# Performance work log

Measured on AMD Instinct MI355X. Metric: run time of the kernel, lower is better.

The kernel has to match this reference:

```python
import jax, jax.numpy as jnp
import numpy as np

EMB_DIM = 64
B, S, D = 64, 1024, 64

def setup_inputs() -> dict:
    key = jax.random.key(0)
    k1, k2, k3, k4, k5 = jax.random.split(key, 5)
    return {
        "query": jax.random.normal(k1, (B, S, D), dtype=jnp.float32),
        "key": jax.random.normal(k2, (B, S, D), dtype=jnp.float32),
        "value": jax.random.normal(k3, (B, S, D), dtype=jnp.float32),
        "a_key": jax.random.normal(k4, (S, S, D), dtype=jnp.float32),
        "a_value": jax.random.normal(k5, (S, S, D), dtype=jnp.float32),
    }

def reference(query, key, value, a_key, a_value):
    scale = jnp.sqrt(jnp.asarray(EMB_DIM, dtype=query.dtype))
    # standard content-content scores: [B, Sq, Sk]
    qk = jnp.einsum("bqd,bkd->bqk", query, key)
    # relative key scores: a_key is [Sq, Sk, D]; contract over D per query position
    rel_qk = jnp.einsum("bqd,qkd->bqk", query, a_key)
    attn = jax.nn.softmax((qk + rel_qk) / scale, axis=-1)
    # content values + relative values
    qkv = jnp.einsum("bqk,bkd->bqd", attn, value)
    rel_qkv = jnp.einsum("bqk,qkd->bqd", attn, a_value)
    return qkv + rel_qkv, attn
```

## Files before the change

kernel.cpp:

```cpp
#include <hip/hip_runtime.h>
#include <stdint.h>

#define S_ 1024
#define D_ 64
#define B_ 64

typedef short short8 __attribute__((ext_vector_type(8)));
typedef unsigned short ushort8 __attribute__((ext_vector_type(8)));
typedef float f32x4 __attribute__((ext_vector_type(4)));
typedef unsigned short u16;

__device__ __forceinline__ u16 f2bf(float x) {
    uint32_t u = __builtin_bit_cast(uint32_t, x);
    return (u16)((u + 0x7FFFu + ((u >> 16) & 1u)) >> 16);
}
__device__ __forceinline__ float bf2f(u16 b) {
    return __builtin_bit_cast(float, ((uint32_t)b) << 16);
}
__device__ __forceinline__ uint32_t pack2(float a, float b) {
    return (uint32_t)f2bf(a) | ((uint32_t)f2bf(b) << 16);
}
__device__ __forceinline__ int scidx(int row, int k) {
    return (((row << 10) + (k & ~7)) ^ ((row & 15) << 3)) + (k & 7);
}

template <int WS>
__global__ __launch_bounds__(256) void k1_qk(const float* __restrict__ Q,
                                             const float* __restrict__ Kk,
                                             float* __restrict__ qkf,
                                             u16* __restrict__ qkb) {
    __shared__ __align__(16) u16 Qs[128][72];
    __shared__ __align__(16) u16 Ks[128][72];
    const float SCL = 0.18033688011112042f;
    const int bx = blockIdx.x;
    const int b  = bx >> 6;
    const int q0 = ((bx >> 3) & 7) << 7;
    const int k0 = (bx & 7) << 7;
    const int t  = threadIdx.x;
#pragma unroll
    for (int i = 0; i < 8; ++i) {
        int f = (i << 8) + t;
        int row = f >> 4, c = (f & 15) << 2;
        float4 v = *reinterpret_cast<const float4*>(&Q[((size_t)(b * S_ + q0 + row) << 6) + c]);
        *reinterpret_cast<uint2*>(&Qs[row][c]) = make_uint2(pack2(v.x, v.y), pack2(v.z, v.w));
        float4 u = *reinterpret_cast<const float4*>(&Kk[((size_t)(b * S_ + k0 + row) << 6) + c]);
        *reinterpret_cast<uint2*>(&Ks[row][c]) = make_uint2(pack2(u.x, u.y), pack2(u.z, u.w));
    }
    __syncthreads();
    const int l = t & 63, w = t >> 6, lr = l & 15, lg = l >> 4;
    short8 a[2][2];
#pragma unroll
    for (int mi = 0; mi < 2; ++mi)
#pragma unroll
        for (int h = 0; h < 2; ++h)
            a[mi][h] = *reinterpret_cast<const short8*>(&Qs[((w * 2 + mi) << 4) + lr][h * 32 + lg * 8]);
    f32x4 acc[2][8] = {};
#pragma unroll
    for (int n = 0; n < 8; ++n) {
        short8 b0 = *reinterpret_cast<const short8*>(&Ks[(n << 4) + lr][lg * 8]);
        short8 b1 = *reinterpret_cast<const short8*>(&Ks[(n << 4) + lr][32 + lg * 8]);
#pragma unroll
        for (int mi = 0; mi < 2; ++mi) {
            acc[mi][n] = __builtin_amdgcn_mfma_f32_16x16x32_bf16(a[mi][0], b0, acc[mi][n], 0, 0, 0);
            acc[mi][n] = __builtin_amdgcn_mfma_f32_16x16x32_bf16(a[mi][1], b1, acc[mi][n], 0, 0, 0);
        }
    }
#pragma unroll
    for (int mi = 0; mi < 2; ++mi)
#pragma unroll
        for (int n = 0; n < 8; ++n)
#pragma unroll
            for (int r = 0; r < 4; ++r) {
                int qq = q0 + ((w * 2 + mi) << 4) + (lg << 2) + r;
                int kc = k0 + (n << 4) + lr;
                size_t idx = ((size_t)(b * S_ + qq) << 10) + kc;
                if (WS) qkb[idx] = f2bf(acc[mi][n][r] * SCL);
                else    qkf[idx] = acc[mi][n][r] * SCL;
            }
}

__device__ __forceinline__ void tpose_store_p(u16* Tls, int pitch, float4 p,
                                              int kb, int t) {
    const int l = t & 63, lr = l & 15, lg = l >> 4;
    float v0 = p.x, v1 = p.y, v2 = p.z, v3 = p.w;
    float y0 = __shfl_xor(v0, 16), y1 = __shfl_xor(v1, 16),
          y2 = __shfl_xor(v2, 16), y3 = __shfl_xor(v3, 16);
    bool o = (lg & 1);
    float n0 = o ? y1 : v0, n1 = o ? v1 : y0, n2 = o ? y3 : v2, n3 = o ? v3 : y2;
    float z0 = __shfl_xor(n0, 32), z1 = __shfl_xor(n1, 32),
          z2 = __shfl_xor(n2, 32), z3 = __shfl_xor(n3, 32);
    bool h = (lg & 2);
    float T0 = h ? z2 : n0, T1 = h ? z3 : n1, T2 = h ? n2 : z0, T3 = h ? n3 : z1;
    int d = (lr << 2) + lg;
    *reinterpret_cast<uint2*>(&Tls[d * pitch + kb]) = make_uint2(pack2(T0, T1), pack2(T2, T3));
}

template <int WS>
__global__ __launch_bounds__(512) void k2_mid(const float* __restrict__ Q,
                                              const float* __restrict__ AK,
                                              const float* __restrict__ AV,
                                              u16* __restrict__ qkb,
                                              const float* __restrict__ qkf,
                                              float* __restrict__ invg,
                                              float* __restrict__ attn,
                                              float* __restrict__ outp) {
    __shared__ __align__(16) u16 Sc[64 * 1024];
    __shared__ __align__(16) u16 Qs[64][72];
    __shared__ __align__(16) u16 Ak[2][64][72];
    __shared__ float invs[64];
    const float SCL = 0.18033688011112042f;
    const int q = blockIdx.x;
    const int t = threadIdx.x;
    const int l = t & 63, w = t >> 6, lr = l & 15, lg = l >> 4;
    const int wq = w & 3;
    const int wh = w >> 2;
    const int srow = t >> 3, sc8 = (t & 7) << 3;

    {
        const float* qp = &Q[((size_t)(srow * S_ + q) << 6) + sc8];
        float4 a = *reinterpret_cast<const float4*>(qp);
        float4 b = *reinterpret_cast<const float4*>(qp + 4);
        *reinterpret_cast<uint4*>(&Qs[srow][sc8]) =
            make_uint4(pack2(a.x * SCL, a.y * SCL), pack2(a.z * SCL, a.w * SCL),
                       pack2(b.x * SCL, b.y * SCL), pack2(b.z * SCL, b.w * SCL));
    }
    const float* akbase = &AK[(size_t)q << 16];
    float4 pa[2][2];
#define LDK(set, tile) do { const float* p_ = akbase + ((size_t)(tile) << 12) + (srow << 6) + sc8; \
        pa[set][0] = *reinterpret_cast<const float4*>(p_);                                         \
        pa[set][1] = *reinterpret_cast<const float4*>(p_ + 4); } while (0)
#define STAGEK(buf) do {                                                                     \
        *reinterpret_cast<uint4*>(&Ak[buf][srow][sc8]) =                                     \
            make_uint4(pack2(pa[buf][0].x, pa[buf][0].y), pack2(pa[buf][0].z, pa[buf][0].w), \
                       pack2(pa[buf][1].x, pa[buf][1].y), pack2(pa[buf][1].z, pa[buf][1].w)); } while (0)
    LDK(0, 0); LDK(1, 1);
    __syncthreads();
    short8 qa[2][2];
#pragma unroll
    for (int bh = 0; bh < 2; ++bh)
#pragma unroll
        for (int h = 0; h < 2; ++h)
            qa[bh][h] = *reinterpret_cast<const short8*>(
                &Qs[(wh << 5) + (bh << 4) + lr][(h << 5) + (lg << 3)]);
    STAGEK(0);
    __syncthreads();

#pragma unroll 2
    for (int tt = 0; tt < 16; ++tt) {
        const int cur = tt & 1, nxt = cur ^ 1;
        short8 ak0 = *reinterpret_cast<const short8*>(&Ak[cur][(wq << 4) + lr][lg << 3]);
        short8 ak1 = *reinterpret_cast<const short8*>(&Ak[cur][(wq << 4) + lr][32 + (lg << 3)]);
        if (tt < 15) STAGEK(nxt);
        if (tt < 14) LDK(cur, tt + 2);
        int kbase = (tt << 6) + (wq << 4) + (lg << 2);
#pragma unroll
        for (int bh = 0; bh < 2; ++bh) {
            f32x4 c = {};
            c = __builtin_amdgcn_mfma_f32_16x16x32_bf16(ak0, qa[bh][0], c, 0, 0, 0);
            c = __builtin_amdgcn_mfma_f32_16x16x32_bf16(ak1, qa[bh][1], c, 0, 0, 0);
            *reinterpret_cast<uint2*>(&Sc[scidx((wh << 5) + (bh << 4) + lr, kbase)]) =
                make_uint2(pack2(c[0], c[1]), pack2(c[2], c[3]));
        }
        __syncthreads();
    }
#undef LDK
#undef STAGEK

    const float* avbase = &AV[(size_t)q << 16];
    float4 pv[2][2];
#pragma unroll
    for (int s = 0; s < 2; ++s)
#pragma unroll
        for (int i = 0; i < 2; ++i) {
            int f = (i << 9) + t;
            pv[s][i] = *reinterpret_cast<const float4*>(
                &avbase[((size_t)s << 12) + ((size_t)(f >> 4) << 6) + ((f & 15) << 2)]);
        }

    {
        const int ch = t & 7;
        float s = 0.f;
#pragma unroll 4
        for (int i = 0; i < 16; ++i) {
            int k = (((i << 3) + ch) << 3);
            int idx = scidx(srow, k);
            ushort8 rel = *reinterpret_cast<const ushort8*>(&Sc[idx]);
            float g[8];
            if (WS) {
                ushort8 gq = *reinterpret_cast<const ushort8*>(
                    &qkb[((size_t)(srow * S_ + q) << 10) + k]);
#pragma unroll
                for (int jj = 0; jj < 8; ++jj) g[jj] = bf2f(gq[jj]);
            } else {
                const float* qkrow = &qkf[((size_t)(srow * S_ + q) << 10)];
                float4 g0 = *reinterpret_cast<const float4*>(&qkrow[k]);
                float4 g1 = *reinterpret_cast<const float4*>(&qkrow[k + 4]);
                g[0] = g0.x; g[1] = g0.y; g[2] = g0.z; g[3] = g0.w;
                g[4] = g1.x; g[5] = g1.y; g[6] = g1.z; g[7] = g1.w;
            }
            ushort8 e;
#pragma unroll
            for (int jj = 0; jj < 8; ++jj) {
                float ev = exp2f(g[jj] + bf2f(rel[jj]));
                s += ev;
                e[jj] = f2bf(ev);
            }
            *reinterpret_cast<ushort8*>(&Sc[idx]) = e;
            if (WS)
                *reinterpret_cast<ushort8*>(&qkb[((size_t)(srow * S_ + q) << 10) + k]) = e;
        }
        s += __shfl_xor(s, 1); s += __shfl_xor(s, 2); s += __shfl_xor(s, 4);
        if (ch == 0) {
            float inv = 1.0f / s;
            invs[srow] = inv;
            if (WS) invg[srow * S_ + q] = inv;
        }
    }
    __syncthreads();

    tpose_store_p(&Ak[0][0][0], 72, pv[0][0], (w << 2), t);
    tpose_store_p(&Ak[0][0][0], 72, pv[0][1], 32 + (w << 2), t);
    __syncthreads();

    f32x4 oacc[2] = {};
#pragma unroll 2
    for (int tt = 0; tt < 16; ++tt) {
        const int cur = tt & 1, nxt = cur ^ 1;
        short8 bb0 = *reinterpret_cast<const short8*>(&Ak[cur][(wq << 4) + lr][lg << 3]);
        short8 bb1 = *reinterpret_cast<const short8*>(&Ak[cur][(wq << 4) + lr][32 + (lg << 3)]);
        if (tt < 15) {
            tpose_store_p(&Ak[nxt][0][0], 72, pv[nxt][0], (w << 2), t);
            tpose_store_p(&Ak[nxt][0][0], 72, pv[nxt][1], 32 + (w << 2), t);
        }
        if (tt < 14) {
#pragma unroll
            for (int i = 0; i < 2; ++i) {
                int f = (i << 9) + t;
                pv[cur][i] = *reinterpret_cast<const float4*>(
                    &avbase[((size_t)(tt + 2) << 12) + ((size_t)(f >> 4) << 6) + ((f & 15) << 2)]);
            }
        }
        {
            int col = (t & 255) << 2;
#pragma unroll
            for (int rr = 0; rr < 2; ++rr) {
                int row = (tt << 2) + (rr << 1) + (t >> 8);
                uint2 u = *reinterpret_cast<const uint2*>(&Sc[scidx(row, col)]);
                float inv = invs[row];
                float4 o = make_float4(bf2f((u16)(u.x & 0xffff)) * inv,
                                       bf2f((u16)(u.x >> 16)) * inv,
                                       bf2f((u16)(u.y & 0xffff)) * inv,
                                       bf2f((u16)(u.y >> 16)) * inv);
                *reinterpret_cast<float4*>(&attn[((size_t)(row * S_ + q) << 10) + col]) = o;
            }
        }
#pragma unroll
        for (int mi = 0; mi < 2; ++mi) {
            short8 ea0 = *reinterpret_cast<const short8*>(
                &Sc[scidx((wh << 5) + (mi << 4) + lr, (tt << 6) + (lg << 3))]);
            short8 ea1 = *reinterpret_cast<const short8*>(
                &Sc[scidx((wh << 5) + (mi << 4) + lr, (tt << 6) + 32 + (lg << 3))]);
            oacc[mi] = __builtin_amdgcn_mfma_f32_16x16x32_bf16(ea0, bb0, oacc[mi], 0, 0, 0);
            oacc[mi] = __builtin_amdgcn_mfma_f32_16x16x32_bf16(ea1, bb1, oacc[mi], 0, 0, 0);
        }
        __syncthreads();
    }
#pragma unroll
    for (int mi = 0; mi < 2; ++mi)
#pragma unroll
        for (int r = 0; r < 4; ++r) {
            int brow = (wh << 5) + (mi << 4) + (lg << 2) + r;
            outp[((size_t)(brow * S_ + q) << 6) + (wq << 4) + lr] = oacc[mi][r] * invs[brow];
        }
}

template <int WS>
__global__ __launch_bounds__(512) void k3_pv(const float* __restrict__ V,
                                             const float* __restrict__ attn,
                                             const u16* __restrict__ P,
                                             const float* __restrict__ invg,
                                             float* __restrict__ outp) {
    __shared__ __align__(16) u16 Vt[64 * 1032];
    __shared__ __align__(16) u16 At[2][64][72];
    const int b  = blockIdx.x >> 2;
    const int qq = blockIdx.x & 3;
    const int t  = threadIdx.x;
    const int l = t & 63, w = t >> 6, lr = l & 15, lg = l >> 4;
    const int wq = w & 3;
    const int dh = w >> 2;
    const int srow = t >> 3, sc8 = (t & 7) << 3;

    for (int kt = 0; kt < 16; ++kt) {
#pragma unroll
        for (int i = 0; i < 2; ++i) {
            int f = (i << 9) + t;
            int row = f >> 4, c = (f & 15) << 2;
            float4 pvv = *reinterpret_cast<const float4*>(
                &V[((size_t)(b * S_ + (kt << 6) + row) << 6) + c]);
            tpose_store_p(&Vt[0], 1032, pvv, (kt << 6) + (i << 5) + (w << 2), t);
        }
    }
    __syncthreads();

    for (int qs = 0; qs < 4; ++qs) {
        const int qsbase = (qq << 8) + (qs << 6);
        f32x4 acc[2] = {};
        if (WS) {
            const u16* prow = &P[((size_t)(b * S_ + qsbase + (wq << 4) + lr) << 10) + (lg << 3)];
            short8 a0b[2], a1b[2];
#define LDPB(buf, kt) do { const u16* p_ = prow + ((kt) << 6);              \
            a0b[buf] = *reinterpret_cast<const short8*>(p_);                \
            a1b[buf] = *reinterpret_cast<const short8*>(p_ + 32); } while (0)
            LDPB(0, 0); LDPB(1, 1);
#pragma unroll 2
            for (int kt = 0; kt < 16; ++kt) {
                const int buf = kt & 1;
                short8 a0 = a0b[buf], a1 = a1b[buf];
                if (kt < 14) LDPB(buf, kt + 2);
#pragma unroll
                for (int n = 0; n < 2; ++n) {
                    const u16* vb = &Vt[((dh << 5) + (n << 4) + lr) * 1032 + (kt << 6) + (lg << 3)];
                    short8 b0 = *reinterpret_cast<const short8*>(vb);
                    short8 b1 = *reinterpret_cast<const short8*>(vb + 32);
                    acc[n] = __builtin_amdgcn_mfma_f32_16x16x32_bf16(a0, b0, acc[n], 0, 0, 0);
                    acc[n] = __builtin_amdgcn_mfma_f32_16x16x32_bf16(a1, b1, acc[n], 0, 0, 0);
                }
            }
#undef LDPB
            float4 inv4 = *reinterpret_cast<const float4*>(
                &invg[b * S_ + qsbase + (wq << 4) + (lg << 2)]);
            float invr[4] = {inv4.x, inv4.y, inv4.z, inv4.w};
#pragma unroll
            for (int n = 0; n < 2; ++n)
#pragma unroll
                for (int r = 0; r < 4; ++r) {
                    size_t idx = ((size_t)(b * S_ + qsbase + (wq << 4) + (lg << 2) + r) << 6)
                                 + (dh << 5) + (n << 4) + lr;
                    outp[idx] += acc[n][r] * invr[r];
                }
        } else {
            const float* arow = &attn[((size_t)(b * S_ + qsbase + srow) << 10) + sc8];
            float4 pa[2][2];
#define LDA3(set, tile) do { const float* p_ = arow + ((tile) << 6);       \
            pa[set][0] = *reinterpret_cast<const float4*>(p_);             \
            pa[set][1] = *reinterpret_cast<const float4*>(p_ + 4); } while (0)
#define STAGEA(buf) do {                                                                     \
            *reinterpret_cast<uint4*>(&At[buf][srow][sc8]) =                                 \
                make_uint4(pack2(pa[buf][0].x, pa[buf][0].y), pack2(pa[buf][0].z, pa[buf][0].w), \
                           pack2(pa[buf][1].x, pa[buf][1].y), pack2(pa[buf][1].z, pa[buf][1].w)); } while (0)
            LDA3(0, 0); LDA3(1, 1);
            __syncthreads();
            STAGEA(0);
            __syncthreads();
#pragma unroll 2
            for (int kt = 0; kt < 16; ++kt) {
                const int cur = kt & 1, nxt = cur ^ 1;
                short8 a0 = *reinterpret_cast<const short8*>(&At[cur][(wq << 4) + lr][lg << 3]);
                short8 a1 = *reinterpret_cast<const short8*>(&At[cur][(wq << 4) + lr][32 + (lg << 3)]);
                if (kt < 15) STAGEA(nxt);
                if (kt < 14) LDA3(cur, kt + 2);
#pragma unroll
                for (int n = 0; n < 2; ++n) {
                    const u16* vb = &Vt[((dh << 5) + (n << 4) + lr) * 1032 + (kt << 6) + (lg << 3)];
                    short8 b0 = *reinterpret_cast<const short8*>(vb);
                    short8 b1 = *reinterpret_cast<const short8*>(vb + 32);
                    acc[n] = __builtin_amdgcn_mfma_f32_16x16x32_bf16(a0, b0, acc[n], 0, 0, 0);
                    acc[n] = __builtin_amdgcn_mfma_f32_16x16x32_bf16(a1, b1, acc[n], 0, 0, 0);
                }
                __syncthreads();
            }
#undef LDA3
#undef STAGEA
#pragma unroll
            for (int n = 0; n < 2; ++n)
#pragma unroll
                for (int r = 0; r < 4; ++r) {
                    size_t idx = ((size_t)(b * S_ + qsbase + (wq << 4) + (lg << 2) + r) << 6)
                                 + (dh << 5) + (n << 4) + lr;
                    outp[idx] += acc[n][r];
                }
        }
    }
}

extern "C" void kernel_launch(void* const* d_in, const int* in_sizes, int n_in,
                              void* d_out, int out_size, void* d_ws, size_t ws_size,
                              hipStream_t stream) {
    (void)in_sizes; (void)n_in; (void)out_size;
    const float* Q  = (const float*)d_in[0];
    const float* K  = (const float*)d_in[1];
    const float* V  = (const float*)d_in[2];
    const float* AK = (const float*)d_in[3];
    const float* AV = (const float*)d_in[4];
    float* outp = (float*)d_out;
    float* attn = outp + (size_t)B_ * S_ * D_;
    u16*   qkb  = (u16*)d_ws;
    float* invg = (float*)(qkb + (size_t)B_ * S_ * S_);
    const size_t need = (size_t)B_ * S_ * S_ * sizeof(u16)
                      + (size_t)B_ * S_ * sizeof(float);

    if (ws_size >= need) {
        k1_qk<1> <<<dim3(64 * 8 * 8), dim3(256), 0, stream>>>(Q, K, attn, qkb);
        k2_mid<1><<<dim3(1024),       dim3(512), 0, stream>>>(Q, AK, AV, qkb, attn, invg, attn, outp);
        k3_pv<1> <<<dim3(256),        dim3(512), 0, stream>>>(V, attn, qkb, invg, outp);
    } else {
        k1_qk<0> <<<dim3(64 * 8 * 8), dim3(256), 0, stream>>>(Q, K, attn, qkb);
        k2_mid<0><<<dim3(1024),       dim3(512), 0, stream>>>(Q, AK, AV, qkb, attn, invg, attn, outp);
        k3_pv<0> <<<dim3(256),        dim3(512), 0, stream>>>(V, attn, qkb, invg, outp);
    }
}
```

Before: 343.7 us.

## Split k2_mid across batch halves with XCD-aware block mapping and smaller blocks

k2_mid now runs 2048 blocks of 256 threads, each handling 32 batch rows for one query position instead of all 64. The block index is remapped so the two blocks sharing a query's a_key/a_value slab land on the same XCD, which should let the second read hit in L2. Shared memory per block is halved and the double-buffered a_key/a_value staging is replaced by a single buffer with an extra sync per tile. This should raise occupancy and spread work more evenly, at the cost of reading each relative-position slab twice and exposing more load latency in the loops.

```diff
diff --git a/kernel.cpp b/kernel.cpp
--- a/kernel.cpp
+++ b/kernel.cpp
@@ -96,7 +96,7 @@
 }
 
 template <int WS>
-__global__ __launch_bounds__(512) void k2_mid(const float* __restrict__ Q,
+__global__ __launch_bounds__(256) void k2_mid(const float* __restrict__ Q,
                                               const float* __restrict__ AK,
                                               const float* __restrict__ AV,
                                               u16* __restrict__ qkb,
@@ -104,20 +104,22 @@
                                               float* __restrict__ invg,
                                               float* __restrict__ attn,
                                               float* __restrict__ outp) {
-    __shared__ __align__(16) u16 Sc[64 * 1024];
-    __shared__ __align__(16) u16 Qs[64][72];
-    __shared__ __align__(16) u16 Ak[2][64][72];
-    __shared__ float invs[64];
+    __shared__ __align__(16) u16 Sc[32 * 1024];
+    __shared__ __align__(16) u16 Qs[32][72];
+    __shared__ __align__(16) u16 Ak[64][72];
+    __shared__ float invs[32];
     const float SCL = 0.18033688011112042f;
-    const int q = blockIdx.x;
+    const int j = blockIdx.x;
+    const int xcd = j & 7, slot = j >> 3;
+    const int q  = xcd * 128 + (slot >> 1);
+    const int b0 = (slot & 1) << 5;
     const int t = threadIdx.x;
     const int l = t & 63, w = t >> 6, lr = l & 15, lg = l >> 4;
-    const int wq = w & 3;
-    const int wh = w >> 2;
     const int srow = t >> 3, sc8 = (t & 7) << 3;
+    const int arow = t >> 2, acol = (t & 3) << 4;
 
     {
-        const float* qp = &Q[((size_t)(srow * S_ + q) << 6) + sc8];
+        const float* qp = &Q[((size_t)((b0 + srow) * S_ + q) << 6) + sc8];
         float4 a = *reinterpret_cast<const float4*>(qp);
         float4 b = *reinterpret_cast<const float4*>(qp + 4);
         *reinterpret_cast<uint4*>(&Qs[srow][sc8]) =
@@ -125,15 +127,20 @@
                        pack2(b.x * SCL, b.y * SCL), pack2(b.z * SCL, b.w * SCL));
     }
     const float* akbase = &AK[(size_t)q << 16];
-    float4 pa[2][2];
-#define LDK(set, tile) do { const float* p_ = akbase + ((size_t)(tile) << 12) + (srow << 6) + sc8; \
-        pa[set][0] = *reinterpret_cast<const float4*>(p_);                                         \
-        pa[set][1] = *reinterpret_cast<const float4*>(p_ + 4); } while (0)
-#define STAGEK(buf) do {                                                                     \
-        *reinterpret_cast<uint4*>(&Ak[buf][srow][sc8]) =                                     \
-            make_uint4(pack2(pa[buf][0].x, pa[buf][0].y), pack2(pa[buf][0].z, pa[buf][0].w), \
-                       pack2(pa[buf][1].x, pa[buf][1].y), pack2(pa[buf][1].z, pa[buf][1].w)); } while (0)
-    LDK(0, 0); LDK(1, 1);
+    float4 pa[4];
+#define LDK(tile) do { const float* p_ = akbase + ((size_t)(tile) << 12) + (arow << 6) + acol; \
+        pa[0] = *reinterpret_cast<const float4*>(p_);                                          \
+        pa[1] = *reinterpret_cast<const float4*>(p_ + 4);                                      \
+        pa[2] = *reinterpret_cast<const float4*>(p_ + 8);                                      \
+        pa[3] = *reinterpret_cast<const float4*>(p_ + 12); } while (0)
+#define STAGEK() do {                                                                        \
+        *reinterpret_cast<uint4*>(&Ak[arow][acol]) =                                         \
+            make_uint4(pack2(pa[0].x, pa[0].y), pack2(pa[0].z, pa[0].w),                     \
+                       pack2(pa[1].x, pa[1].y), pack2(pa[1].z, pa[1].w));                    \
+        *reinterpret_cast<uint4*>(&Ak[arow][acol + 8]) =                                     \
+            make_uint4(pack2(pa[2].x, pa[2].y), pack2(pa[2].z, pa[2].w),                     \
+                       pack2(pa[3].x, pa[3].y), pack2(pa[3].z, pa[3].w)); } while (0)
+    LDK(0);
     __syncthreads();
     short8 qa[2][2];
 #pragma unroll
@@ -141,24 +148,21 @@
 #pragma unroll
         for (int h = 0; h < 2; ++h)
             qa[bh][h] = *reinterpret_cast<const short8*>(
-                &Qs[(wh << 5) + (bh << 4) + lr][(h << 5) + (lg << 3)]);
-    STAGEK(0);
-    __syncthreads();
-
-#pragma unroll 2
+                &Qs[(bh << 4) + lr][(h << 5) + (lg << 3)]);
+
     for (int tt = 0; tt < 16; ++tt) {
-        const int cur = tt & 1, nxt = cur ^ 1;
-        short8 ak0 = *reinterpret_cast<const short8*>(&Ak[cur][(wq << 4) + lr][lg << 3]);
-        short8 ak1 = *reinterpret_cast<const short8*>(&Ak[cur][(wq << 4) + lr][32 + (lg << 3)]);
-        if (tt < 15) STAGEK(nxt);
-        if (tt < 14) LDK(cur, tt + 2);
-        int kbase = (tt << 6) + (wq << 4) + (lg << 2);
+        STAGEK();
+        __syncthreads();
+        if (tt < 15) LDK(tt + 1);
+        short8 ak0 = *reinterpret_cast<const short8*>(&Ak[(w << 4) + lr][lg << 3]);
+        short8 ak1 = *reinterpret_cast<const short8*>(&Ak[(w << 4) + lr][32 + (lg << 3)]);
+        int kbase = (tt << 6) + (w << 4) + (lg << 2);
 #pragma unroll
         for (int bh = 0; bh < 2; ++bh) {
             f32x4 c = {};
             c = __builtin_amdgcn_mfma_f32_16x16x32_bf16(ak0, qa[bh][0], c, 0, 0, 0);
             c = __builtin_amdgcn_mfma_f32_16x16x32_bf16(ak1, qa[bh][1], c, 0, 0, 0);
-            *reinterpret_cast<uint2*>(&Sc[scidx((wh << 5) + (bh << 4) + lr, kbase)]) =
+            *reinterpret_cast<uint2*>(&Sc[scidx((bh << 4) + lr, kbase)]) =
                 make_uint2(pack2(c[0], c[1]), pack2(c[2], c[3]));
         }
         __syncthreads();
@@ -167,15 +171,13 @@
 #undef STAGEK
 
     const float* avbase = &AV[(size_t)q << 16];
-    float4 pv[2][2];
-#pragma unroll
-    for (int s = 0; s < 2; ++s)
-#pragma unroll
-        for (int i = 0; i < 2; ++i) {
-            int f = (i << 9) + t;
-            pv[s][i] = *reinterpret_cast<const float4*>(
-                &avbase[((size_t)s << 12) + ((size_t)(f >> 4) << 6) + ((f & 15) << 2)]);
-        }
+    float4 pv[4];
+#pragma unroll
+    for (int i = 0; i < 4; ++i) {
+        int f = (i << 8) + t;
+        pv[i] = *reinterpret_cast<const float4*>(
+            &avbase[((size_t)(f >> 4) << 6) + ((f & 15) << 2)]);
+    }
 
     {
         const int ch = t & 7;
@@ -188,11 +190,11 @@
             float g[8];
             if (WS) {
                 ushort8 gq = *reinterpret_cast<const ushort8*>(
-                    &qkb[((size_t)(srow * S_ + q) << 10) + k]);
+                    &qkb[((size_t)((b0 + srow) * S_ + q) << 10) + k]);
 #pragma unroll
                 for (int jj = 0; jj < 8; ++jj) g[jj] = bf2f(gq[jj]);
             } else {
-                const float* qkrow = &qkf[((size_t)(srow * S_ + q) << 10)];
+                const float* qkrow = &qkf[((size_t)((b0 + srow) * S_ + q) << 10)];
                 float4 g0 = *reinterpret_cast<const float4*>(&qkrow[k]);
                 float4 g1 = *reinterpret_cast<const float4*>(&qkrow[k + 4]);
                 g[0] = g0.x; g[1] = g0.y; g[2] = g0.z; g[3] = g0.w;
@@ -207,59 +209,53 @@
             }
             *reinterpret_cast<ushort8*>(&Sc[idx]) = e;
             if (WS)
-                *reinterpret_cast<ushort8*>(&qkb[((size_t)(srow * S_ + q) << 10) + k]) = e;
+                *reinterpret_cast<ushort8*>(&qkb[((size_t)((b0 + srow) * S_ + q) << 10) + k]) = e;
         }
         s += __shfl_xor(s, 1); s += __shfl_xor(s, 2); s += __shfl_xor(s, 4);
         if (ch == 0) {
             float inv = 1.0f / s;
             invs[srow] = inv;
-            if (WS) invg[srow * S_ + q] = inv;
+            if (WS) invg[(b0 + srow) * S_ + q] = inv;
         }
     }
     __syncthreads();
 
-    tpose_store_p(&Ak[0][0][0], 72, pv[0][0], (w << 2), t);
-    tpose_store_p(&Ak[0][0][0], 72, pv[0][1], 32 + (w << 2), t);
-    __syncthreads();
-
     f32x4 oacc[2] = {};
-#pragma unroll 2
     for (int tt = 0; tt < 16; ++tt) {
-        const int cur = tt & 1, nxt = cur ^ 1;
-        short8 bb0 = *reinterpret_cast<const short8*>(&Ak[cur][(wq << 4) + lr][lg << 3]);
-        short8 bb1 = *reinterpret_cast<const short8*>(&Ak[cur][(wq << 4) + lr][32 + (lg << 3)]);
+#pragma unroll
+        for (int i = 0; i < 4; ++i)
+            tpose_store_p(&Ak[0][0], 72, pv[i], (i << 4) + (w << 2), t);
+        __syncthreads();
         if (tt < 15) {
-            tpose_store_p(&Ak[nxt][0][0], 72, pv[nxt][0], (w << 2), t);
-            tpose_store_p(&Ak[nxt][0][0], 72, pv[nxt][1], 32 + (w << 2), t);
-        }
-        if (tt < 14) {
-#pragma unroll
-            for (int i = 0; i < 2; ++i) {
-                int f = (i << 9) + t;
-                pv[cur][i] = *reinterpret_cast<const float4*>(
-                    &avbase[((size_t)(tt + 2) << 12) + ((size_t)(f >> 4) << 6) + ((f & 15) << 2)]);
+#pragma unroll
+            for (int i = 0; i < 4; ++i) {
+                int f = (i << 8) + t;
+                pv[i] = *reinterpret_cast<const float4*>(
+                    &avbase[((size_t)(tt + 1) << 12) + ((size_t)(f >> 4) << 6) + ((f & 15) << 2)]);
             }
         }
         {
-            int col = (t & 255) << 2;
+            int col = t << 2;
 #pragma unroll
             for (int rr = 0; rr < 2; ++rr) {
-                int row = (tt << 2) + (rr << 1) + (t >> 8);
+                int row = (tt << 1) + rr;
                 uint2 u = *reinterpret_cast<const uint2*>(&Sc[scidx(row, col)]);
                 float inv = invs[row];
                 float4 o = make_float4(bf2f((u16)(u.x & 0xffff)) * inv,
                                        bf2f((u16)(u.x >> 16)) * inv,
                                        bf2f((u16)(u.y & 0xffff)) * inv,
                                        bf2f((u16)(u.y >> 16)) * inv);
-                *reinterpret_cast<float4*>(&attn[((size_t)(row * S_ + q) << 10) + col]) = o;
-            }
-        }
+                *reinterpret_cast<float4*>(&attn[((size_t)((b0 + row) * S_ + q) << 10) + col]) = o;
+            }
+        }
+        short8 bb0 = *reinterpret_cast<const short8*>(&Ak[(w << 4) + lr][lg << 3]);
+        short8 bb1 = *reinterpret_cast<const short8*>(&Ak[(w << 4) + lr][32 + (lg << 3)]);
 #pragma unroll
         for (int mi = 0; mi < 2; ++mi) {
             short8 ea0 = *reinterpret_cast<const short8*>(
-                &Sc[scidx((wh << 5) + (mi << 4) + lr, (tt << 6) + (lg << 3))]);
+                &Sc[scidx((mi << 4) + lr, (tt << 6) + (lg << 3))]);
             short8 ea1 = *reinterpret_cast<const short8*>(
-                &Sc[scidx((wh << 5) + (mi << 4) + lr, (tt << 6) + 32 + (lg << 3))]);
+                &Sc[scidx((mi << 4) + lr, (tt << 6) + 32 + (lg << 3))]);
             oacc[mi] = __builtin_amdgcn_mfma_f32_16x16x32_bf16(ea0, bb0, oacc[mi], 0, 0, 0);
             oacc[mi] = __builtin_amdgcn_mfma_f32_16x16x32_bf16(ea1, bb1, oacc[mi], 0, 0, 0);
         }
@@ -269,8 +265,8 @@
     for (int mi = 0; mi < 2; ++mi)
 #pragma unroll
         for (int r = 0; r < 4; ++r) {
-            int brow = (wh << 5) + (mi << 4) + (lg << 2) + r;
-            outp[((size_t)(brow * S_ + q) << 6) + (wq << 4) + lr] = oacc[mi][r] * invs[brow];
+            int brow = (mi << 4) + (lg << 2) + r;
+            outp[((size_t)((b0 + brow) * S_ + q) << 6) + (w << 4) + lr] = oacc[mi][r] * invs[brow];
         }
 }
 
@@ -401,11 +397,11 @@
 
     if (ws_size >= need) {
         k1_qk<1> <<<dim3(64 * 8 * 8), dim3(256), 0, stream>>>(Q, K, attn, qkb);
-        k2_mid<1><<<dim3(1024),       dim3(512), 0, stream>>>(Q, AK, AV, qkb, attn, invg, attn, outp);
+        k2_mid<1><<<dim3(2048),       dim3(256), 0, stream>>>(Q, AK, AV, qkb, attn, invg, attn, outp);
         k3_pv<1> <<<dim3(256),        dim3(512), 0, stream>>>(V, attn, qkb, invg, outp);
     } else {
         k1_qk<0> <<<dim3(64 * 8 * 8), dim3(256), 0, stream>>>(Q, K, attn, qkb);
-        k2_mid<0><<<dim3(1024),       dim3(512), 0, stream>>>(Q, AK, AV, qkb, attn, invg, attn, outp);
+        k2_mid<0><<<dim3(2048),       dim3(256), 0, stream>>>(Q, AK, AV, qkb, attn, invg, attn, outp);
         k3_pv<0> <<<dim3(256),        dim3(512), 0, stream>>>(V, attn, qkb, invg, outp);
     }
 }
```

Result: slower. 370.3 us (+7.7%).

## Stream a_key tiles into LDS via async global_load_lds triple buffer

Applied to the files above, without the earlier changes.

Replaces the register-staged, bf16-converted double buffer for the a_key scores phase with direct global-to-LDS async loads (global_load_lds) into a swizzled fp32 triple buffer, synchronized with explicit vmcnt waits and raw barriers. Q fragments are now loaded straight from global into registers instead of going through shared memory, and the wave-to-work mapping changes to 32 key rows per step. This aims to remove the register round trip and keep more loads in flight, in exchange for fp32 data in LDS, bf16 conversion after the LDS read, and fragile hand-written waitcnt/barrier synchronization.

```diff
diff --git a/kernel.cpp b/kernel.cpp
--- a/kernel.cpp
+++ b/kernel.cpp
@@ -19,6 +19,17 @@
 }
 __device__ __forceinline__ uint32_t pack2(float a, float b) {
     return (uint32_t)f2bf(a) | ((uint32_t)f2bf(b) << 16);
+}
+__device__ __forceinline__ short8 mkfrag(float4 a, float4 b) {
+    union { short8 s; uint32_t u[4]; } r;
+    r.u[0] = pack2(a.x, a.y); r.u[1] = pack2(a.z, a.w);
+    r.u[2] = pack2(b.x, b.y); r.u[3] = pack2(b.z, b.w);
+    return r.s;
+}
+__device__ __forceinline__ void gload16(const float* src, float* ldst) {
+    __builtin_amdgcn_global_load_lds(
+        (const __attribute__((address_space(1))) void*)src,
+        (__attribute__((address_space(3))) void*)ldst, 16, 0, 0);
 }
 __device__ __forceinline__ int scidx(int row, int k) {
     return (((row << 10) + (k & ~7)) ^ ((row & 15) << 3)) + (k & 7);
@@ -105,66 +116,76 @@
                                               float* __restrict__ attn,
                                               float* __restrict__ outp) {
     __shared__ __align__(16) u16 Sc[64 * 1024];
-    __shared__ __align__(16) u16 Qs[64][72];
-    __shared__ __align__(16) u16 Ak[2][64][72];
+    __shared__ __align__(16) unsigned char Ureg[24576];
     __shared__ float invs[64];
+    float* HF  = reinterpret_cast<float*>(Ureg);
+    u16*   Akb = reinterpret_cast<u16*>(Ureg);
     const float SCL = 0.18033688011112042f;
     const int q = blockIdx.x;
     const int t = threadIdx.x;
     const int l = t & 63, w = t >> 6, lr = l & 15, lg = l >> 4;
     const int wq = w & 3;
     const int wh = w >> 2;
-    const int srow = t >> 3, sc8 = (t & 7) << 3;
-
+    const int kg = w & 1;
+    const int bg = w >> 1;
+    const int srow = t >> 3;
+
+    const float* akbase = &AK[(size_t)q << 16];
+    const int gl = (w << 6) + l;
+    const int grow = gl >> 4, ggc = gl & 15;
+    const float* dsrc = akbase + (grow << 6) + ((ggc ^ (grow & 7)) << 2);
+    float* ldst = HF + (w << 8);
+
+    gload16(dsrc,            ldst);
+    gload16(dsrc + 2048,     ldst + 2048);
+    gload16(dsrc + 4096,     ldst + 4096);
+
+    short8 qa0, qa1;
     {
-        const float* qp = &Q[((size_t)(srow * S_ + q) << 6) + sc8];
+        const float* qp = &Q[((size_t)(((bg << 4) + lr) * S_ + q) << 6) + (lg << 3)];
         float4 a = *reinterpret_cast<const float4*>(qp);
         float4 b = *reinterpret_cast<const float4*>(qp + 4);
-        *reinterpret_cast<uint4*>(&Qs[srow][sc8]) =
-            make_uint4(pack2(a.x * SCL, a.y * SCL), pack2(a.z * SCL, a.w * SCL),
-                       pack2(b.x * SCL, b.y * SCL), pack2(b.z * SCL, b.w * SCL));
-    }
-    const float* akbase = &AK[(size_t)q << 16];
-    float4 pa[2][2];
-#define LDK(set, tile) do { const float* p_ = akbase + ((size_t)(tile) << 12) + (srow << 6) + sc8; \
-        pa[set][0] = *reinterpret_cast<const float4*>(p_);                                         \
-        pa[set][1] = *reinterpret_cast<const float4*>(p_ + 4); } while (0)
-#define STAGEK(buf) do {                                                                     \
-        *reinterpret_cast<uint4*>(&Ak[buf][srow][sc8]) =                                     \
-            make_uint4(pack2(pa[buf][0].x, pa[buf][0].y), pack2(pa[buf][0].z, pa[buf][0].w), \
-                       pack2(pa[buf][1].x, pa[buf][1].y), pack2(pa[buf][1].z, pa[buf][1].w)); } while (0)
-    LDK(0, 0); LDK(1, 1);
-    __syncthreads();
-    short8 qa[2][2];
-#pragma unroll
-    for (int bh = 0; bh < 2; ++bh)
-#pragma unroll
-        for (int h = 0; h < 2; ++h)
-            qa[bh][h] = *reinterpret_cast<const short8*>(
-                &Qs[(wh << 5) + (bh << 4) + lr][(h << 5) + (lg << 3)]);
-    STAGEK(0);
-    __syncthreads();
-
-#pragma unroll 2
-    for (int tt = 0; tt < 16; ++tt) {
-        const int cur = tt & 1, nxt = cur ^ 1;
-        short8 ak0 = *reinterpret_cast<const short8*>(&Ak[cur][(wq << 4) + lr][lg << 3]);
-        short8 ak1 = *reinterpret_cast<const short8*>(&Ak[cur][(wq << 4) + lr][32 + (lg << 3)]);
-        if (tt < 15) STAGEK(nxt);
-        if (tt < 14) LDK(cur, tt + 2);
-        int kbase = (tt << 6) + (wq << 4) + (lg << 2);
-#pragma unroll
-        for (int bh = 0; bh < 2; ++bh) {
+        float4 c2 = *reinterpret_cast<const float4*>(qp + 32);
+        float4 d2 = *reinterpret_cast<const float4*>(qp + 36);
+        a.x *= SCL; a.y *= SCL; a.z *= SCL; a.w *= SCL;
+        b.x *= SCL; b.y *= SCL; b.z *= SCL; b.w *= SCL;
+        c2.x *= SCL; c2.y *= SCL; c2.z *= SCL; c2.w *= SCL;
+        d2.x *= SCL; d2.y *= SCL; d2.z *= SCL; d2.w *= SCL;
+        qa0 = mkfrag(a, b);
+        qa1 = mkfrag(c2, d2);
+    }
+
+    {
+        const int r = (kg << 4) + lr;
+        const int sg = r & 7;
+        const float* rowb;
+#pragma unroll
+        for (int h = 0; h < 32; ++h) {
+            if (h < 30)       asm volatile("s_waitcnt vmcnt(2)" ::: "memory");
+            else if (h == 30) asm volatile("s_waitcnt vmcnt(1)" ::: "memory");
+            else              asm volatile("s_waitcnt vmcnt(0)" ::: "memory");
+            __builtin_amdgcn_sched_barrier(0);
+            __builtin_amdgcn_s_barrier();
+            rowb = HF + (h % 3) * 2048 + (r << 6);
+            float4 r0 = *reinterpret_cast<const float4*>(rowb + ((((lg << 1) + 0) ^ sg) << 2));
+            float4 r1 = *reinterpret_cast<const float4*>(rowb + ((((lg << 1) + 1) ^ sg) << 2));
+            float4 r2 = *reinterpret_cast<const float4*>(rowb + ((((lg << 1) + 8) ^ sg) << 2));
+            float4 r3 = *reinterpret_cast<const float4*>(rowb + ((((lg << 1) + 9) ^ sg) << 2));
+            short8 ak0 = mkfrag(r0, r1);
+            short8 ak1 = mkfrag(r2, r3);
             f32x4 c = {};
-            c = __builtin_amdgcn_mfma_f32_16x16x32_bf16(ak0, qa[bh][0], c, 0, 0, 0);
-            c = __builtin_amdgcn_mfma_f32_16x16x32_bf16(ak1, qa[bh][1], c, 0, 0, 0);
-            *reinterpret_cast<uint2*>(&Sc[scidx((wh << 5) + (bh << 4) + lr, kbase)]) =
+            c = __builtin_amdgcn_mfma_f32_16x16x32_bf16(ak0, qa0, c, 0, 0, 0);
+            c = __builtin_amdgcn_mfma_f32_16x16x32_bf16(ak1, qa1, c, 0, 0, 0);
+            int kbase = (h << 5) + (kg << 4) + (lg << 2);
+            *reinterpret_cast<uint2*>(&Sc[scidx((bg << 4) + lr, kbase)]) =
                 make_uint2(pack2(c[0], c[1]), pack2(c[2], c[3]));
-        }
-        __syncthreads();
-    }
-#undef LDK
-#undef STAGEK
+            asm volatile("s_waitcnt lgkmcnt(0)" ::: "memory");
+            __builtin_amdgcn_sched_barrier(0);
+            __builtin_amdgcn_s_barrier();
+            if (h + 3 < 32)
+                gload16(dsrc + (size_t)(h + 3) * 2048, HF + ((h + 3) % 3) * 2048 + (w << 8));
+        }
+    }
 
     const float* avbase = &AV[(size_t)q << 16];
     float4 pv[2][2];
@@ -218,19 +239,20 @@
     }
     __syncthreads();
 
-    tpose_store_p(&Ak[0][0][0], 72, pv[0][0], (w << 2), t);
-    tpose_store_p(&Ak[0][0][0], 72, pv[0][1], 32 + (w << 2), t);
+    tpose_store_p(Akb, 72, pv[0][0], (w << 2), t);
+    tpose_store_p(Akb, 72, pv[0][1], 32 + (w << 2), t);
     __syncthreads();
 
     f32x4 oacc[2] = {};
 #pragma unroll 2
     for (int tt = 0; tt < 16; ++tt) {
         const int cur = tt & 1, nxt = cur ^ 1;
-        short8 bb0 = *reinterpret_cast<const short8*>(&Ak[cur][(wq << 4) + lr][lg << 3]);
-        short8 bb1 = *reinterpret_cast<const short8*>(&Ak[cur][(wq << 4) + lr][32 + (lg << 3)]);
+        const u16* Akc = Akb + cur * 4608;
+        short8 bb0 = *reinterpret_cast<const short8*>(&Akc[((wq << 4) + lr) * 72 + (lg << 3)]);
+        short8 bb1 = *reinterpret_cast<const short8*>(&Akc[((wq << 4) + lr) * 72 + 32 + (lg << 3)]);
         if (tt < 15) {
-            tpose_store_p(&Ak[nxt][0][0], 72, pv[nxt][0], (w << 2), t);
-            tpose_store_p(&Ak[nxt][0][0], 72, pv[nxt][1], 32 + (w << 2), t);
+            tpose_store_p(Akb + nxt * 4608, 72, pv[nxt][0], (w << 2), t);
+            tpose_store_p(Akb + nxt * 4608, 72, pv[nxt][1], 32 + (w << 2), t);
         }
         if (tt < 14) {
 #pragma unroll
```

Result: slower. 370.3 us (+7.7%).
